# Kernel tuning notes

Hardware: AMD Instinct MI355X
Metric: run time of the kernel (lower is better)

## Reference

```python
import jax, jax.numpy as jnp
import numpy as np

LEAKY_SLOPE = 0.2  # LeakyReLU(0.2) attention activation from the torch module
HEADS = 4
RATES = (10, 25)


def _prod(v):
    r = 1
    for x in v:
        r *= x
    return r


def gat_conv(x_self, x_neigh, W, a_s, a_n):
    """Single GAT aggregation layer (aggregate_method='concat').
    x_self:  [..., F_in]
    x_neigh: [..., E, F_in] (leading dims reshape-compatible with x_self)
    W: [F_in, H*D], a_s/a_n: [H, D]
    Returns [..., H*D].
    """
    H = HEADS
    D = W.shape[1] // H
    lead = x_self.shape[:-1]
    E = x_neigh.shape[-2]
    z_s = (x_self @ W).reshape(lead + (H, D))                  # [..., H, D]
    z_n = (x_neigh @ W).reshape(lead + (E, H, D))              # [..., E, H, D]
    e_s = jnp.einsum('...hd,hd->...h', z_s, a_s)               # [..., H]
    e_n = jnp.einsum('...ehd,hd->...eh', z_n, a_n)             # [..., E, H]
    logits = jax.nn.leaky_relu(e_s[..., None, :] + e_n, LEAKY_SLOPE)
    alpha = jax.nn.softmax(logits, axis=-2)                    # softmax over neighbors E
    out = jnp.einsum('...eh,...ehd->...hd', alpha, z_n)        # attention-weighted sum
    return out.reshape(lead + (H * D,))


def setup_inputs() -> dict:
    key = jax.random.key(0)
    ks = jax.random.split(key, 10)
    B, F, HID, OUT = 1024, 128, 512, 256
    s = 0.05
    return {
        'h0': jax.random.normal(ks[0], (B, F), jnp.float32),
        'h1': jax.random.normal(ks[1], (B, RATES[0], F), jnp.float32),
        'h2': jax.random.normal(ks[2], (B, RATES[0] * RATES[1], F), jnp.float32),
        'W0': jax.random.normal(ks[3], (F, HID), jnp.float32) * s,
        'a0_s': jax.random.normal(ks[4], (HEADS, HID // HEADS), jnp.float32) * s,
        'a0_n': jax.random.normal(ks[5], (HEADS, HID // HEADS), jnp.float32) * s,
        'W1': jax.random.normal(ks[6], (HID, HID), jnp.float32) * s,
        'a1_s': jax.random.normal(ks[7], (HEADS, HID // HEADS), jnp.float32) * s,
        'a1_n': jax.random.normal(ks[8], (HEADS, HID // HEADS), jnp.float32) * s,
        'W_fc': jax.random.normal(ks[9], (HID, OUT), jnp.float32) * s,
    }


def reference(h0, h1, h2, W0, a0_s, a0_n, W1, a1_s, a1_n, W_fc):
    B = h0.shape[0]
    hs = [h0, h1, h2]
    layers = [(W0, a0_s, a0_n), (W1, a1_s, a1_n)]
    depth = len(RATES)
    # hierarchical sweep: layer i is applied to levels 0..depth-i-1
    for i, (W, a_s, a_n) in enumerate(layers):
        for j in range(depth - i):
            x_self = hs[j]
            x_neigh = hs[j + 1].reshape(B, _prod(RATES[:j]), RATES[j], -1)
            hs[j] = gat_conv(x_self, x_neigh, W, a_s, a_n)
    return hs[0] @ W_fc  # final Linear (no bias, no activation)
```

## Files before the change

kernel.cpp:

```cpp
#include <hip/hip_runtime.h>

__device__ __forceinline__ void gemm_body(
    float* __restrict__ smem,
    const float* __restrict__ A, int lda,
    const float* __restrict__ B, int ldb,
    float* __restrict__ C, int ldc, int K,
    int m0, int col0) {
  float* As = smem;
  float* Bs = smem + 16 * 68;
  const int t = threadIdx.x;
  const int tn = t & 31, tm = t >> 5;
  const int lam = t >> 2, lak = (t & 3) * 4;
  const int lbk = t >> 4, lbn = (t & 15) * 8;
  float acc[8][4];
#pragma unroll
  for (int i = 0; i < 8; ++i)
#pragma unroll
    for (int j = 0; j < 4; ++j) acc[i][j] = 0.f;
  for (int k0 = 0; k0 < K; k0 += 16) {
    float4 av = *reinterpret_cast<const float4*>(A + (size_t)(m0 + lam) * lda + k0 + lak);
    As[(lak + 0) * 68 + lam] = av.x;
    As[(lak + 1) * 68 + lam] = av.y;
    As[(lak + 2) * 68 + lam] = av.z;
    As[(lak + 3) * 68 + lam] = av.w;
    const float* bp = B + (size_t)(k0 + lbk) * ldb + col0 + lbn;
    float4 b0 = *reinterpret_cast<const float4*>(bp);
    float4 b1 = *reinterpret_cast<const float4*>(bp + 4);
    float* bd = &Bs[lbk * 132 + lbn];
    bd[0] = b0.x; bd[1] = b0.y; bd[2] = b0.z; bd[3] = b0.w;
    bd[4] = b1.x; bd[5] = b1.y; bd[6] = b1.z; bd[7] = b1.w;
    __syncthreads();
#pragma unroll
    for (int kk = 0; kk < 16; ++kk) {
      float4 a0 = *reinterpret_cast<const float4*>(&As[kk * 68 + tm * 8]);
      float4 a1 = *reinterpret_cast<const float4*>(&As[kk * 68 + tm * 8 + 4]);
      float4 bv = *reinterpret_cast<const float4*>(&Bs[kk * 132 + tn * 4]);
      float a[8] = {a0.x, a0.y, a0.z, a0.w, a1.x, a1.y, a1.z, a1.w};
      float b[4] = {bv.x, bv.y, bv.z, bv.w};
#pragma unroll
      for (int i = 0; i < 8; ++i)
#pragma unroll
        for (int j = 0; j < 4; ++j) acc[i][j] = fmaf(a[i], b[j], acc[i][j]);
    }
    __syncthreads();
  }
#pragma unroll
  for (int i = 0; i < 8; ++i) {
    float* cp = C + (size_t)(m0 + tm * 8 + i) * ldc + col0 + tn * 4;
    *reinterpret_cast<float4*>(cp) =
        make_float4(acc[i][0], acc[i][1], acc[i][2], acc[i][3]);
  }
}

template <int FIN, int TPR, int E>
__device__ __forceinline__ void gat_body(
    float* __restrict__ smem,
    const float* __restrict__ xself, const float* __restrict__ xneigh,
    const float* __restrict__ waS, const float* __restrict__ waN,
    float* __restrict__ out) {
  constexpr int MR = E + 1;
  constexpr int RPP = 256 / TPR;
  constexpr int PSTR = TPR + 1;
  constexpr int G = TPR / 4;
  float* tile = smem;
  float* partial = tile + MR * FIN;
  float* logitS = partial + MR * PSTR;
  float* alpha = logitS + MR * 4;
  const int t = threadIdx.x;
  const int el = t / TPR;
  const int f0 = (t % TPR) * 4;
  float4 wn[4], ws[4];
#pragma unroll
  for (int h = 0; h < 4; ++h) {
    wn[h] = *reinterpret_cast<const float4*>(waN + h * FIN + f0);
    ws[h] = *reinterpret_cast<const float4*>(waS + h * FIN + f0);
  }
#pragma unroll
  for (int p = 0; p * RPP < MR; ++p) {
    int e = p * RPP + el;
    if (e < MR) {
      const float* src = (e < E) ? (xneigh + (size_t)e * FIN + f0) : (xself + f0);
      float4 x = *reinterpret_cast<const float4*>(src);
      *reinterpret_cast<float4*>(tile + e * FIN + f0) = x;
      float ph[4];
#pragma unroll
      for (int h = 0; h < 4; ++h) {
        float4 w = (e < E) ? wn[h] : ws[h];
        ph[h] = x.x * w.x + x.y * w.y + x.z * w.z + x.w * w.w;
      }
#pragma unroll
      for (int h = 0; h < 4; ++h) {
        ph[h] += __shfl_xor(ph[h], 1);
        ph[h] += __shfl_xor(ph[h], 2);
      }
      if ((t & 3) == 0) {
        int g = (t % TPR) >> 2;
        *reinterpret_cast<float4*>(partial + e * PSTR + g * 4) =
            make_float4(ph[0], ph[1], ph[2], ph[3]);
      }
    }
  }
  __syncthreads();
  if (t < MR * 4) {
    int e = t >> 2, h = t & 3;
    float v = 0.f;
#pragma unroll
    for (int g = 0; g < G; ++g) v += partial[e * PSTR + g * 4 + h];
    logitS[t] = v;
  }
  __syncthreads();
  if (t < 4) {
    const float es = logitS[E * 4 + t];
    float m = -1e30f;
#pragma unroll
    for (int e = 0; e < E; ++e) {
      float x = es + logitS[e * 4 + t];
      x = (x > 0.f) ? x : 0.2f * x;
      m = fmaxf(m, x);
    }
    float s = 0.f;
#pragma unroll
    for (int e = 0; e < E; ++e) {
      float x = es + logitS[e * 4 + t];
      x = (x > 0.f) ? x : 0.2f * x;
      float p = __expf(x - m);
      alpha[e * 4 + t] = p;
      s += p;
    }
    float inv = 1.f / s;
#pragma unroll
    for (int e = 0; e < E; ++e) alpha[e * 4 + t] *= inv;
  }
  __syncthreads();
  constexpr int C = FIN / 4;
  for (int o = t; o < 4 * C; o += 256) {
    int h = o / C, f = (o % C) * 4;
    float4 acc = make_float4(0.f, 0.f, 0.f, 0.f);
#pragma unroll
    for (int e = 0; e < E; ++e) {
      float a = alpha[e * 4 + h];
      float4 x = *reinterpret_cast<const float4*>(tile + e * FIN + f);
      acc.x = fmaf(a, x.x, acc.x);
      acc.y = fmaf(a, x.y, acc.y);
      acc.z = fmaf(a, x.z, acc.z);
      acc.w = fmaf(a, x.w, acc.w);
    }
    *reinterpret_cast<float4*>(out + h * FIN + f) = acc;
  }
}

__global__ void __launch_bounds__(256) prepA(
    const float* __restrict__ W0, const float* __restrict__ a0s,
    const float* __restrict__ a0n,
    const float* __restrict__ W1, const float* __restrict__ a1s,
    const float* __restrict__ a1n, const float* __restrict__ Wfc,
    float* __restrict__ wa0s, float* __restrict__ wa0n,
    float* __restrict__ wa1s, float* __restrict__ wa1n,
    float* __restrict__ T) {
  __shared__ float smem[3200];
  const int b = blockIdx.x;
  if (b < 64) {
    int h = b >> 4, mb = (b >> 1) & 7, nb = b & 1;
    gemm_body(smem, W1 + h * 128, 512, Wfc + (size_t)h * 32768, 256,
              T + (size_t)h * 131072, 256, 128, mb * 64, nb * 128);
    return;
  }
  int idx = (b - 64) * 256 + threadIdx.x;
  if (idx >= 5120) return;
  const float* W; const float* a; float* dst; int i; int FIN;
  if (idx < 512)       { W = W0; a = a0s; dst = wa0s; i = idx;        FIN = 128; }
  else if (idx < 1024) { W = W0; a = a0n; dst = wa0n; i = idx - 512;  FIN = 128; }
  else if (idx < 3072) { W = W1; a = a1s; dst = wa1s; i = idx - 1024; FIN = 512; }
  else                 { W = W1; a = a1n; dst = wa1n; i = idx - 3072; FIN = 512; }
  int f = i >> 2, h = i & 3;
  const float* wrow = W + (size_t)f * 512 + h * 128;
  const float* arow = a + h * 128;
  float v = 0.f;
#pragma unroll 8
  for (int d = 0; d < 128; ++d) v = fmaf(wrow[d], arow[d], v);
  dst[h * FIN + f] = v;
}

__global__ void __launch_bounds__(256) fusedB(
    const float* __restrict__ h0, const float* __restrict__ h1,
    const float* __restrict__ h2, const float* __restrict__ wa0s,
    const float* __restrict__ wa0n, float* __restrict__ xagg,
    const float* __restrict__ W0, const float* __restrict__ wa1s,
    const float* __restrict__ wa1n, const float* __restrict__ T,
    float* __restrict__ va1s, float* __restrict__ va1n,
    float* __restrict__ Wfinal) {
  __shared__ float smem[4390];
  const int b = blockIdx.x;
  if (b < 1024) {
    gat_body<128, 32, 10>(smem, h0 + (size_t)b * 128, h1 + (size_t)b * 1280,
                          wa0s, wa0n, xagg + (size_t)b * 512);
    return;
  }
  if (b < 11264) {
    int g = b - 1024;
    gat_body<128, 32, 25>(smem, h1 + (size_t)g * 128, h2 + (size_t)g * 3200,
                          wa0s, wa0n, xagg + (size_t)b * 512);
    return;
  }
  if (b < 11264 + 64) {
    int g = b - 11264;
    int pair = g >> 2, mb = (g >> 1) & 1, nb = g & 1;
    int h = pair >> 2, h0b = pair & 3;
    gemm_body(smem, W0 + h0b * 128, 512,
              T + (size_t)h * 131072 + (size_t)h0b * 32768, 256,
              Wfinal + (size_t)h * 131072 + (size_t)h0b * 32768, 256, 128,
              mb * 64, nb * 128);
    return;
  }
  int idx = (b - 11328) * 256 + threadIdx.x;
  if (idx >= 4096) return;
  const float* wa = (idx < 2048) ? wa1s : wa1n;
  float* dst = (idx < 2048) ? va1s : va1n;
  int i = idx & 2047;
  int h = i >> 9, h0b = (i >> 7) & 3, f = i & 127;
  const float* w0row = W0 + (size_t)f * 512 + h0b * 128;
  const float* warow = wa + h * 512 + h0b * 128;
  float v = 0.f;
#pragma unroll 8
  for (int n = 0; n < 128; ++n) v = fmaf(w0row[n], warow[n], v);
  dst[i] = v;
}

__global__ void __launch_bounds__(256) gat_layer1(
    const float* __restrict__ xagg, const float* __restrict__ vaS,
    const float* __restrict__ vaN, float* __restrict__ aggx) {
  __shared__ float smem[7135];
  const int b = blockIdx.x;
  gat_body<512, 128, 10>(smem, xagg + (size_t)b * 512,
                         xagg + (size_t)(1024 + b * 10) * 512, vaS, vaN,
                         aggx + (size_t)b * 2048);
}

__global__ void __launch_bounds__(256) gemm_ksplit(
    const float* __restrict__ A, const float* __restrict__ B,
    float* __restrict__ Cpart) {
  __shared__ float smem[3200];
  const int ks = blockIdx.z;
  gemm_body(smem, A + ks * 256, 2048, B + (size_t)ks * 65536, 256,
            Cpart + (size_t)ks * 262144, 256, 256, blockIdx.x * 64,
            blockIdx.y * 128);
}

__global__ void __launch_bounds__(256) reduce8(
    const float* __restrict__ Cpart, float* __restrict__ out) {
  int i = blockIdx.x * 256 + threadIdx.x;
  const float4* p = reinterpret_cast<const float4*>(Cpart) + i;
  float4 s = p[0];
#pragma unroll
  for (int ks = 1; ks < 8; ++ks) {
    float4 v = p[(size_t)ks * 65536];
    s.x += v.x; s.y += v.y; s.z += v.z; s.w += v.w;
  }
  reinterpret_cast<float4*>(out)[i] = s;
}

extern "C" void kernel_launch(void* const* d_in, const int* in_sizes, int n_in,
                              void* d_out, int out_size, void* d_ws, size_t ws_size,
                              hipStream_t stream) {
  const float* h0  = (const float*)d_in[0];
  const float* h1  = (const float*)d_in[1];
  const float* h2  = (const float*)d_in[2];
  const float* W0  = (const float*)d_in[3];
  const float* a0s = (const float*)d_in[4];
  const float* a0n = (const float*)d_in[5];
  const float* W1  = (const float*)d_in[6];
  const float* a1s = (const float*)d_in[7];
  const float* a1n = (const float*)d_in[8];
  const float* Wfc = (const float*)d_in[9];
  float* out = (float*)d_out;

  float* ws = (float*)d_ws;
  float* wa0s   = ws;
  float* wa0n   = wa0s + 512;
  float* wa1s   = wa0n + 512;
  float* wa1n   = wa1s + 2048;
  float* va1s   = wa1n + 2048;
  float* va1n   = va1s + 2048;
  float* T      = va1n + 2048;
  float* Wfinal = T + 524288;
  float* xaggA  = Wfinal + 524288;
  float* aggx   = xaggA + 11264 * 512;
  float* Cpart  = aggx + 2097152;

  prepA<<<84, 256, 0, stream>>>(W0, a0s, a0n, W1, a1s, a1n, Wfc,
                                wa0s, wa0n, wa1s, wa1n, T);
  fusedB<<<11344, 256, 0, stream>>>(h0, h1, h2, wa0s, wa0n, xaggA,
                                    W0, wa1s, wa1n, T, va1s, va1n, Wfinal);
  gat_layer1<<<1024, 256, 0, stream>>>(xaggA, va1s, va1n, aggx);
  gemm_ksplit<<<dim3(16, 2, 8), 256, 0, stream>>>(aggx, Wfinal, Cpart);
  reduce8<<<256, 256, 0, stream>>>(Cpart, out);
}
```

Before: 269.9 us.

## Keep neighbor rows in registers and reduce attention output via partial sums

The GAT body no longer stages the full neighbor tile in shared memory. Each thread keeps its loaded rows in registers, accumulates alpha-weighted per-head sums locally, combines pairs with a cross-half-wave shuffle, and writes small partials that a final pass sums. This cuts shared-memory footprint and traffic, and adds launch-bounds occupancy hints of four blocks per SM for the fused and layer-1 kernels. In exchange it adds register pressure plus an extra shared-memory reduction step and barrier.

Result: no change. 273.2 us (+1.2%).

```diff
diff --git a/kernel.cpp b/kernel.cpp
--- a/kernel.cpp
+++ b/kernel.cpp
@@ -60,28 +60,32 @@
     float* __restrict__ out) {
   constexpr int MR = E + 1;
   constexpr int RPP = 256 / TPR;
-  constexpr int PSTR = TPR + 1;
+  constexpr int P = (MR + RPP - 1) / RPP;
+  constexpr int PSTR = TPR + 4;
   constexpr int G = TPR / 4;
-  float* tile = smem;
-  float* partial = tile + MR * FIN;
+  constexpr int WG = (TPR == 32) ? RPP / 2 : RPP;
+  float* part2 = smem;
+  float* partial = part2 + WG * 4 * FIN;
   float* logitS = partial + MR * PSTR;
   float* alpha = logitS + MR * 4;
   const int t = threadIdx.x;
   const int el = t / TPR;
-  const int f0 = (t % TPR) * 4;
+  const int fl = t % TPR;
+  const int f0 = fl * 4;
   float4 wn[4], ws[4];
 #pragma unroll
   for (int h = 0; h < 4; ++h) {
     wn[h] = *reinterpret_cast<const float4*>(waN + h * FIN + f0);
     ws[h] = *reinterpret_cast<const float4*>(waS + h * FIN + f0);
   }
-#pragma unroll
-  for (int p = 0; p * RPP < MR; ++p) {
+  float4 xr[P];
+#pragma unroll
+  for (int p = 0; p < P; ++p) {
     int e = p * RPP + el;
     if (e < MR) {
       const float* src = (e < E) ? (xneigh + (size_t)e * FIN + f0) : (xself + f0);
       float4 x = *reinterpret_cast<const float4*>(src);
-      *reinterpret_cast<float4*>(tile + e * FIN + f0) = x;
+      xr[p] = x;
       float ph[4];
 #pragma unroll
       for (int h = 0; h < 4; ++h) {
@@ -94,7 +98,7 @@
         ph[h] += __shfl_xor(ph[h], 2);
       }
       if ((t & 3) == 0) {
-        int g = (t % TPR) >> 2;
+        int g = fl >> 2;
         *reinterpret_cast<float4*>(partial + e * PSTR + g * 4) =
             make_float4(ph[0], ph[1], ph[2], ph[3]);
       }
@@ -132,18 +136,52 @@
     for (int e = 0; e < E; ++e) alpha[e * 4 + t] *= inv;
   }
   __syncthreads();
+  float4 racc[4];
+#pragma unroll
+  for (int h = 0; h < 4; ++h) racc[h] = make_float4(0.f, 0.f, 0.f, 0.f);
+#pragma unroll
+  for (int p = 0; p < P; ++p) {
+    int e = p * RPP + el;
+    if (e < E) {
+      float4 x = xr[p];
+#pragma unroll
+      for (int h = 0; h < 4; ++h) {
+        float a = alpha[e * 4 + h];
+        racc[h].x = fmaf(a, x.x, racc[h].x);
+        racc[h].y = fmaf(a, x.y, racc[h].y);
+        racc[h].z = fmaf(a, x.z, racc[h].z);
+        racc[h].w = fmaf(a, x.w, racc[h].w);
+      }
+    }
+  }
+  if constexpr (TPR == 32) {
+#pragma unroll
+    for (int h = 0; h < 4; ++h) {
+      racc[h].x += __shfl_xor(racc[h].x, 32);
+      racc[h].y += __shfl_xor(racc[h].y, 32);
+      racc[h].z += __shfl_xor(racc[h].z, 32);
+      racc[h].w += __shfl_xor(racc[h].w, 32);
+    }
+    if ((t & 32) == 0) {
+      int g = t >> 6;
+#pragma unroll
+      for (int h = 0; h < 4; ++h)
+        *reinterpret_cast<float4*>(part2 + (g * 4 + h) * FIN + f0) = racc[h];
+    }
+  } else {
+#pragma unroll
+    for (int h = 0; h < 4; ++h)
+      *reinterpret_cast<float4*>(part2 + (el * 4 + h) * FIN + f0) = racc[h];
+  }
+  __syncthreads();
   constexpr int C = FIN / 4;
-  for (int o = t; o < 4 * C; o += 256) {
+  for (int o = t; o < FIN; o += 256) {
     int h = o / C, f = (o % C) * 4;
     float4 acc = make_float4(0.f, 0.f, 0.f, 0.f);
 #pragma unroll
-    for (int e = 0; e < E; ++e) {
-      float a = alpha[e * 4 + h];
-      float4 x = *reinterpret_cast<const float4*>(tile + e * FIN + f);
-      acc.x = fmaf(a, x.x, acc.x);
-      acc.y = fmaf(a, x.y, acc.y);
-      acc.z = fmaf(a, x.z, acc.z);
-      acc.w = fmaf(a, x.w, acc.w);
+    for (int g = 0; g < WG; ++g) {
+      float4 v = *reinterpret_cast<const float4*>(part2 + (g * 4 + h) * FIN + f);
+      acc.x += v.x; acc.y += v.y; acc.z += v.z; acc.w += v.w;
     }
     *reinterpret_cast<float4*>(out + h * FIN + f) = acc;
   }
@@ -181,7 +219,7 @@
   dst[h * FIN + f] = v;
 }
 
-__global__ void __launch_bounds__(256) fusedB(
+__global__ void __launch_bounds__(256, 4) fusedB(
     const float* __restrict__ h0, const float* __restrict__ h1,
     const float* __restrict__ h2, const float* __restrict__ wa0s,
     const float* __restrict__ wa0n, float* __restrict__ xagg,
@@ -189,7 +227,7 @@
     const float* __restrict__ wa1n, const float* __restrict__ T,
     float* __restrict__ va1s, float* __restrict__ va1n,
     float* __restrict__ Wfinal) {
-  __shared__ float smem[4390];
+  __shared__ float smem[3200];
   const int b = blockIdx.x;
   if (b < 1024) {
     gat_body<128, 32, 10>(smem, h0 + (size_t)b * 128, h1 + (size_t)b * 1280,
@@ -226,10 +264,10 @@
   dst[i] = v;
 }
 
-__global__ void __launch_bounds__(256) gat_layer1(
+__global__ void __launch_bounds__(256, 4) gat_layer1(
     const float* __restrict__ xagg, const float* __restrict__ vaS,
     const float* __restrict__ vaN, float* __restrict__ aggx) {
-  __shared__ float smem[7135];
+  __shared__ float smem[5632];
   const int b = blockIdx.x;
   gat_body<512, 128, 10>(smem, xagg + (size_t)b * 512,
                          xagg + (size_t)(1024 + b * 10) * 512, vaS, vaN,
```

## Fuse per-root GAT subtree into one kernel keeping layer-0 outputs in LDS

Applied to the files above, without the earlier changes.

Replaces the large fused layer-0 kernel and the separate layer-1 GAT kernel with one 'subtree' kernel. Each block processes one root: its 10 child GAT aggregations and the root aggregation, with all 11 layer-0 outputs held in shared memory, then runs layer-1 attention directly. This removes the 23 MB global round-trip of the intermediate xagg buffer and one kernel launch. The va1 projection precompute moves into prepA. In exchange the launch drops from about 11k small blocks to about 1k serialized blocks that use more LDS, so occupancy and latency hiding may suffer.

Result: slower. 317.1 us (+17.5%).

```diff
diff --git a/kernel.cpp b/kernel.cpp
--- a/kernel.cpp
+++ b/kernel.cpp
@@ -52,29 +52,20 @@
   }
 }
 
-template <int FIN, int TPR, int E>
-__device__ __forceinline__ void gat_body(
-    float* __restrict__ smem,
+template <int E>
+__device__ __forceinline__ void gat_small(
+    float* __restrict__ scratch,
     const float* __restrict__ xself, const float* __restrict__ xneigh,
-    const float* __restrict__ waS, const float* __restrict__ waN,
+    const float4* __restrict__ wn, const float4* __restrict__ ws,
     float* __restrict__ out) {
-  constexpr int MR = E + 1;
-  constexpr int RPP = 256 / TPR;
-  constexpr int PSTR = TPR + 1;
-  constexpr int G = TPR / 4;
-  float* tile = smem;
+  constexpr int FIN = 128, MR = E + 1, RPP = 8, PSTR = 33, G = 8;
+  float* tile = scratch;
   float* partial = tile + MR * FIN;
   float* logitS = partial + MR * PSTR;
   float* alpha = logitS + MR * 4;
   const int t = threadIdx.x;
-  const int el = t / TPR;
-  const int f0 = (t % TPR) * 4;
-  float4 wn[4], ws[4];
-#pragma unroll
-  for (int h = 0; h < 4; ++h) {
-    wn[h] = *reinterpret_cast<const float4*>(waN + h * FIN + f0);
-    ws[h] = *reinterpret_cast<const float4*>(waS + h * FIN + f0);
-  }
+  const int el = t >> 5;
+  const int f0 = (t & 31) * 4;
 #pragma unroll
   for (int p = 0; p * RPP < MR; ++p) {
     int e = p * RPP + el;
@@ -94,8 +85,7 @@
         ph[h] += __shfl_xor(ph[h], 2);
       }
       if ((t & 3) == 0) {
-        int g = (t % TPR) >> 2;
-        *reinterpret_cast<float4*>(partial + e * PSTR + g * 4) =
+        *reinterpret_cast<float4*>(partial + e * PSTR + ((t & 31) >> 2) * 4) =
             make_float4(ph[0], ph[1], ph[2], ph[3]);
       }
     }
@@ -132,9 +122,8 @@
     for (int e = 0; e < E; ++e) alpha[e * 4 + t] *= inv;
   }
   __syncthreads();
-  constexpr int C = FIN / 4;
-  for (int o = t; o < 4 * C; o += 256) {
-    int h = o / C, f = (o % C) * 4;
+  if (t < 128) {
+    int h = t >> 5, f = (t & 31) * 4;
     float4 acc = make_float4(0.f, 0.f, 0.f, 0.f);
 #pragma unroll
     for (int e = 0; e < E; ++e) {
@@ -155,55 +144,70 @@
     const float* __restrict__ W1, const float* __restrict__ a1s,
     const float* __restrict__ a1n, const float* __restrict__ Wfc,
     float* __restrict__ wa0s, float* __restrict__ wa0n,
-    float* __restrict__ wa1s, float* __restrict__ wa1n,
+    float* __restrict__ va1s, float* __restrict__ va1n,
     float* __restrict__ T) {
   __shared__ float smem[3200];
   const int b = blockIdx.x;
+  const int t = threadIdx.x;
   if (b < 64) {
     int h = b >> 4, mb = (b >> 1) & 7, nb = b & 1;
     gemm_body(smem, W1 + h * 128, 512, Wfc + (size_t)h * 32768, 256,
               T + (size_t)h * 131072, 256, 128, mb * 64, nb * 128);
     return;
   }
-  int idx = (b - 64) * 256 + threadIdx.x;
-  if (idx >= 5120) return;
-  const float* W; const float* a; float* dst; int i; int FIN;
-  if (idx < 512)       { W = W0; a = a0s; dst = wa0s; i = idx;        FIN = 128; }
-  else if (idx < 1024) { W = W0; a = a0n; dst = wa0n; i = idx - 512;  FIN = 128; }
-  else if (idx < 3072) { W = W1; a = a1s; dst = wa1s; i = idx - 1024; FIN = 512; }
-  else                 { W = W1; a = a1n; dst = wa1n; i = idx - 3072; FIN = 512; }
-  int f = i >> 2, h = i & 3;
-  const float* wrow = W + (size_t)f * 512 + h * 128;
-  const float* arow = a + h * 128;
-  float v = 0.f;
+  if (b < 68) {
+    int idx = (b - 64) * 256 + t;
+    const float* a = (idx < 512) ? a0s : a0n;
+    float* dst = (idx < 512) ? wa0s : wa0n;
+    int i = idx & 511;
+    int f = i >> 2, h = i & 3;
+    const float* wrow = W0 + (size_t)f * 512 + h * 128;
+    const float* arow = a + h * 128;
+    float v = 0.f;
 #pragma unroll 8
-  for (int d = 0; d < 128; ++d) v = fmaf(wrow[d], arow[d], v);
-  dst[h * FIN + f] = v;
-}
-
-__global__ void __launch_bounds__(256) fusedB(
+    for (int d = 0; d < 128; ++d) v = fmaf(wrow[d], arow[d], v);
+    dst[h * 128 + f] = v;
+    return;
+  }
+  int v = b - 68;
+  int sel = v >> 3, h = (v >> 1) & 3, hp = v & 1;
+  const float* a1 = sel ? a1n : a1s;
+  float* dst = sel ? va1n : va1s;
+  int h0b = hp * 2 + (t >> 7);
+  float* ws1 = smem;
+  {
+    int n = t & 127;
+    const float* w1row = W1 + (size_t)(h0b * 128 + n) * 512 + h * 128;
+    const float* arow = a1 + h * 128;
+    float s = 0.f;
+#pragma unroll 8
+    for (int d = 0; d < 128; ++d) s = fmaf(w1row[d], arow[d], s);
+    ws1[t] = s;
+  }
+  __syncthreads();
+  {
+    int f = t & 127;
+    const float* w0row = W0 + (size_t)f * 512 + h0b * 128;
+    const float* wsl = ws1 + (t >> 7) * 128;
+    float s = 0.f;
+#pragma unroll 8
+    for (int n = 0; n < 128; ++n) s = fmaf(w0row[n], wsl[n], s);
+    dst[h * 512 + h0b * 128 + f] = s;
+  }
+}
+
+__global__ void __launch_bounds__(256, 4) subtree(
     const float* __restrict__ h0, const float* __restrict__ h1,
-    const float* __restrict__ h2, const float* __restrict__ wa0s,
-    const float* __restrict__ wa0n, float* __restrict__ xagg,
-    const float* __restrict__ W0, const float* __restrict__ wa1s,
-    const float* __restrict__ wa1n, const float* __restrict__ T,
-    float* __restrict__ va1s, float* __restrict__ va1n,
-    float* __restrict__ Wfinal) {
-  __shared__ float smem[4390];
-  const int b = blockIdx.x;
-  if (b < 1024) {
-    gat_body<128, 32, 10>(smem, h0 + (size_t)b * 128, h1 + (size_t)b * 1280,
-                          wa0s, wa0n, xagg + (size_t)b * 512);
-    return;
-  }
-  if (b < 11264) {
-    int g = b - 1024;
-    gat_body<128, 32, 25>(smem, h1 + (size_t)g * 128, h2 + (size_t)g * 3200,
-                          wa0s, wa0n, xagg + (size_t)b * 512);
-    return;
-  }
-  if (b < 11264 + 64) {
-    int g = b - 11264;
+    const float* __restrict__ h2,
+    const float* __restrict__ wa0s, const float* __restrict__ wa0n,
+    const float* __restrict__ va1s, const float* __restrict__ va1n,
+    const float* __restrict__ W0, const float* __restrict__ T,
+    float* __restrict__ Wfinal, float* __restrict__ aggx) {
+  __shared__ float smem[10022];
+  const int b0 = blockIdx.x;
+  const int t = threadIdx.x;
+  if (b0 < 64) {
+    int g = b0;
     int pair = g >> 2, mb = (g >> 1) & 1, nb = g & 1;
     int h = pair >> 2, h0b = pair & 3;
     gemm_body(smem, W0 + h0b * 128, 512,
@@ -212,28 +216,110 @@
               mb * 64, nb * 128);
     return;
   }
-  int idx = (b - 11328) * 256 + threadIdx.x;
-  if (idx >= 4096) return;
-  const float* wa = (idx < 2048) ? wa1s : wa1n;
-  float* dst = (idx < 2048) ? va1s : va1n;
-  int i = idx & 2047;
-  int h = i >> 9, h0b = (i >> 7) & 3, f = i & 127;
-  const float* w0row = W0 + (size_t)f * 512 + h0b * 128;
-  const float* warow = wa + h * 512 + h0b * 128;
-  float v = 0.f;
-#pragma unroll 8
-  for (int n = 0; n < 128; ++n) v = fmaf(w0row[n], warow[n], v);
-  dst[i] = v;
-}
-
-__global__ void __launch_bounds__(256) gat_layer1(
-    const float* __restrict__ xagg, const float* __restrict__ vaS,
-    const float* __restrict__ vaN, float* __restrict__ aggx) {
-  __shared__ float smem[7135];
-  const int b = blockIdx.x;
-  gat_body<512, 128, 10>(smem, xagg + (size_t)b * 512,
-                         xagg + (size_t)(1024 + b * 10) * 512, vaS, vaN,
-                         aggx + (size_t)b * 2048);
+  const int b = b0 - 64;
+  float* xaggL = smem;
+  float* scratch = smem + 5632;
+  {
+    const int f0 = (t & 31) * 4;
+    float4 wn[4], ws4[4];
+#pragma unroll
+    for (int h = 0; h < 4; ++h) {
+      wn[h] = *reinterpret_cast<const float4*>(wa0n + h * 128 + f0);
+      ws4[h] = *reinterpret_cast<const float4*>(wa0s + h * 128 + f0);
+    }
+    gat_small<10>(scratch, h0 + (size_t)b * 128, h1 + (size_t)b * 1280,
+                  wn, ws4, xaggL + 10 * 512);
+    __syncthreads();
+#pragma unroll 1
+    for (int c = 0; c < 10; ++c) {
+      gat_small<25>(scratch, h1 + (size_t)(b * 10 + c) * 128,
+                    h2 + (size_t)(b * 10 + c) * 3200, wn, ws4, xaggL + c * 512);
+      __syncthreads();
+    }
+  }
+  {
+    constexpr int PSTR = 129;
+    float* partial = scratch;
+    float* logitS = partial + 11 * PSTR;
+    float* alpha = logitS + 44;
+    const int el = t >> 7;
+    const int f0 = (t & 127) * 4;
+    float4 vn[4], vs4[4];
+#pragma unroll
+    for (int h = 0; h < 4; ++h) {
+      vn[h] = *reinterpret_cast<const float4*>(va1n + h * 512 + f0);
+      vs4[h] = *reinterpret_cast<const float4*>(va1s + h * 512 + f0);
+    }
+#pragma unroll
+    for (int p = 0; p < 6; ++p) {
+      int e = p * 2 + el;
+      if (e < 11) {
+        float4 x = *reinterpret_cast<const float4*>(xaggL + e * 512 + f0);
+        float ph[4];
+#pragma unroll
+        for (int h = 0; h < 4; ++h) {
+          float4 w = (e < 10) ? vn[h] : vs4[h];
+          ph[h] = x.x * w.x + x.y * w.y + x.z * w.z + x.w * w.w;
+        }
+#pragma unroll
+        for (int h = 0; h < 4; ++h) {
+          ph[h] += __shfl_xor(ph[h], 1);
+          ph[h] += __shfl_xor(ph[h], 2);
+        }
+        if ((t & 3) == 0) {
+          *reinterpret_cast<float4*>(partial + e * PSTR + ((t & 127) >> 2) * 4) =
+              make_float4(ph[0], ph[1], ph[2], ph[3]);
+        }
+      }
+    }
+    __syncthreads();
+    if (t < 44) {
+      int e = t >> 2, h = t & 3;
+      float v = 0.f;
+#pragma unroll
+      for (int g = 0; g < 32; ++g) v += partial[e * PSTR + g * 4 + h];
+      logitS[t] = v;
+    }
+    __syncthreads();
+    if (t < 4) {
+      const float es = logitS[10 * 4 + t];
+      float m = -1e30f;
+#pragma unroll
+      for (int e = 0; e < 10; ++e) {
+        float x = es + logitS[e * 4 + t];
+        x = (x > 0.f) ? x : 0.2f * x;
+        m = fmaxf(m, x);
+      }
+      float s = 0.f;
+#pragma unroll
+      for (int e = 0; e < 10; ++e) {
+        float x = es + logitS[e * 4 + t];
+        x = (x > 0.f) ? x : 0.2f * x;
+        float p = __expf(x - m);
+        alpha[e * 4 + t] = p;
+        s += p;
+      }
+      float inv = 1.f / s;
+#pragma unroll
+      for (int e = 0; e < 10; ++e) alpha[e * 4 + t] *= inv;
+    }
+    __syncthreads();
+    float* outb = aggx + (size_t)b * 2048;
+    for (int o = t; o < 512; o += 256) {
+      int h = o >> 7, f = (o & 127) * 4;
+      float4 acc = make_float4(0.f, 0.f, 0.f, 0.f);
+#pragma unroll
+      for (int e = 0; e < 10; ++e) {
+        float a = alpha[e * 4 + h];
+        float4 x = *reinterpret_cast<const float4*>(xaggL + e * 512 + f);
+        acc.x = fmaf(a, x.x, acc.x);
+        acc.y = fmaf(a, x.y, acc.y);
+        acc.z = fmaf(a, x.z, acc.z);
+        acc.w = fmaf(a, x.w, acc.w);
+      }
+      *reinterpret_cast<float4*>(outb + h * 512 + f) = acc;
+    }
+  }
 }
 
 __global__ void __launch_bounds__(256) gemm_ksplit(
@@ -277,21 +363,17 @@
   float* ws = (float*)d_ws;
   float* wa0s   = ws;
   float* wa0n   = wa0s + 512;
-  float* wa1s   = wa0n + 512;
-  float* wa1n   = wa1s + 2048;
-  float* va1s   = wa1n + 2048;
+  float* va1s   = wa0n + 512;
   float* va1n   = va1s + 2048;
   float* T      = va1n + 2048;
   float* Wfinal = T + 524288;
-  float* xaggA  = Wfinal + 524288;
-  float* aggx   = xaggA + 11264 * 512;
+  float* aggx   = Wfinal + 524288;
   float* Cpart  = aggx + 2097152;
 
   prepA<<<84, 256, 0, stream>>>(W0, a0s, a0n, W1, a1s, a1n, Wfc,
-                                wa0s, wa0n, wa1s, wa1n, T);
-  fusedB<<<11344, 256, 0, stream>>>(h0, h1, h2, wa0s, wa0n, xaggA,
-                                    W0, wa1s, wa1n, T, va1s, va1n, Wfinal);
-  gat_layer1<<<1024, 256, 0, stream>>>(xaggA, va1s, va1n, aggx);
+                                wa0s, wa0n, va1s, va1n, T);
+  subtree<<<1088, 256, 0, stream>>>(h0, h1, h2, wa0s, wa0n, va1s, va1n,
+                                    W0, T, Wfinal, aggx);
   gemm_ksplit<<<dim3(16, 2, 8), 256, 0, stream>>>(aggx, Wfinal, Cpart);
   reduce8<<<256, 256, 0, stream>>>(Cpart, out);
 }
```
